# Optimization experiments

Measured on AMD Instinct MI355X. Metric: run time of the kernel, lower is better.

The kernel has to match this reference:

```python
import jax, jax.numpy as jnp
import numpy as np
import math

ALPHA = 0.5


def _dfrft_matrix(N: int, a: float) -> np.ndarray:
    """Candan's discrete fractional Fourier transform matrix (approx order 2),
    as used by torch-frft's dfrft. D(a) = E diag(exp(-i*pi/2*a*k)) E^T, where E
    are eigenvectors (even/odd interleaved, descending eigenvalue) of the
    S = circulant([0,1,0,...,0,1]) + diag(Re fft(s)) matrix that commutes with the DFT.
    Pure numpy; runs at trace time (constants)."""
    s = np.zeros(N)
    s[1] = 1.0
    s[-1] = 1.0
    idx = (np.arange(N)[:, None] - np.arange(N)[None, :]) % N
    S = s[idx] + np.diag(np.fft.fft(s).real)
    # odd/even decomposition matrix P (orthogonal)
    r = N // 2
    even = 1 - (N % 2)
    P = np.zeros((N, N))
    P[0, 0] = 1.0
    c = 1.0 / math.sqrt(2.0)
    for i in range(1, r - even + 1):
        P[i, i] = c
        P[i, N - i] = c
    if even:
        P[r, r] = 1.0
    for i in range(r + 1, N):
        P[i, i] = -c
        P[i, N - i] = c
    CS = P @ S @ P.T
    C2 = CS[: r + 1, : r + 1]
    S2 = CS[r + 1:, r + 1:]
    _, vc = np.linalg.eigh(C2)  # ascending -> reverse for descending order
    _, vs = np.linalg.eigh(S2)
    SC2 = (P @ np.vstack((vc, np.zeros((N - r - 1, r + 1)))))[:, ::-1]  # even evecs
    SS2 = (P @ np.vstack((np.zeros((r + 1, N - r - 1)), vs)))[:, ::-1]  # odd evecs
    if N % 2 == 0:
        E = np.zeros((N, N + 1))
        E[:, 0::2] = SC2
        E[:, 1::2] = np.hstack((SS2, np.zeros((N, 1))))
        E = np.delete(E, N - 1, axis=1)  # skip eigenvalue index N-1, keep N
    else:
        E = np.zeros((N, N))
        E[:, 0::2] = SC2
        E[:, 1::2] = SS2
    shift = 1 - (N % 2)
    k = np.concatenate((np.arange(N - 1), [N - 1 + shift]))
    f = np.exp(-1j * (np.pi / 2.0) * a * k)
    return (E * f[None, :]) @ E.T


def setup_inputs() -> dict:
    key = jax.random.key(0)
    k1, k2, k3, k4, k5 = jax.random.split(key, 5)
    B, Ci, Co, H, W = 16, 64, 64, 128, 128
    scale = 1.0 / Ci
    return {
        "x": jax.random.normal(k1, (B, Ci, H, W), jnp.float32),
        "w_r": jax.random.normal(k2, (Co, Ci), jnp.float32) * scale,
        "w_i": jax.random.normal(k3, (Co, Ci), jnp.float32) * scale,
        "b_r": jax.random.normal(k4, (Co,), jnp.float32) * scale,
        "b_i": jax.random.normal(k5, (Co,), jnp.float32) * scale,
    }


def reference(x, w_r, w_i, b_r, b_i):
    B, Ci, H, W = x.shape
    Aw = jnp.asarray(_dfrft_matrix(W, ALPHA), jnp.complex64)   # dfrft along dim=-1
    Ah = jnp.asarray(_dfrft_matrix(H, ALPHA), jnp.complex64)   # dfrft along dim=-2
    xc = x.astype(jnp.complex64)
    # forward fractional Fourier transforms
    x_ft = jnp.einsum('wv,bchv->bchw', Aw, xc)
    x_ft = jnp.einsum('hg,bcgw->bchw', Ah, x_ft)
    # 1x1 complex conv (complex weight + bias)
    wc = w_r.astype(jnp.complex64) + 1j * w_i.astype(jnp.complex64)
    bc = b_r.astype(jnp.complex64) + 1j * b_i.astype(jnp.complex64)
    out_ft = jnp.einsum('oi,bihw->bohw', wc, x_ft) + bc[None, :, None, None]
    # inverse transforms: D(-a) = conj(D(a)) since eigenvectors are real
    y = jnp.einsum('hg,bogw->bohw', jnp.conj(Ah), out_ft)
    y = jnp.einsum('wv,bohv->bohw', jnp.conj(Aw), y)
    # module returns a complex tensor; expose as stacked (real, imag)
    return jnp.stack((y.real, y.imag), axis=0)
```

## Files before the change

kernel.cpp:

```cpp
#include <hip/hip_runtime.h>
#include <cmath>
#include <cstring>
#include <vector>
#include <algorithm>


struct UV { float ur[128]; float ui[128]; };
static UV g_uv;

namespace {

constexpr int NN = 128;

void matmul_d(const std::vector<double>& A, const std::vector<double>& B,
              std::vector<double>& C, int n) {
  for (int i = 0; i < n; ++i)
    for (int j = 0; j < n; ++j) {
      double s = 0.0;
      for (int k = 0; k < n; ++k) s += A[(size_t)i*n+k] * B[(size_t)k*n+j];
      C[(size_t)i*n+j] = s;
    }
}

void jacobi_eigh(std::vector<double>& A, int n, std::vector<double>& V,
                 std::vector<double>& lam) {
  V.assign((size_t)n*n, 0.0);
  for (int i = 0; i < n; ++i) V[(size_t)i*n+i] = 1.0;
  for (int sweep = 0; sweep < 200; ++sweep) {
    double off = 0.0;
    for (int p = 0; p < n; ++p)
      for (int q = p+1; q < n; ++q) off += A[(size_t)p*n+q]*A[(size_t)p*n+q];
    if (off < 1e-24) break;
    for (int p = 0; p < n-1; ++p)
      for (int q = p+1; q < n; ++q) {
        double apq = A[(size_t)p*n+q];
        if (std::fabs(apq) < 1e-300) continue;
        double app = A[(size_t)p*n+p], aqq = A[(size_t)q*n+q];
        double tau = (aqq - app) / (2.0*apq);
        double t = (tau >= 0 ? 1.0 : -1.0) / (std::fabs(tau) + std::sqrt(1.0 + tau*tau));
        double c = 1.0/std::sqrt(1.0 + t*t), s = t*c;
        for (int k = 0; k < n; ++k) {
          double akp = A[(size_t)k*n+p], akq = A[(size_t)k*n+q];
          A[(size_t)k*n+p] = c*akp - s*akq;
          A[(size_t)k*n+q] = s*akp + c*akq;
        }
        for (int k = 0; k < n; ++k) {
          double apk = A[(size_t)p*n+k], aqk = A[(size_t)q*n+k];
          A[(size_t)p*n+k] = c*apk - s*aqk;
          A[(size_t)q*n+k] = s*apk + c*aqk;
        }
        for (int k = 0; k < n; ++k) {
          double vkp = V[(size_t)k*n+p], vkq = V[(size_t)k*n+q];
          V[(size_t)k*n+p] = c*vkp - s*vkq;
          V[(size_t)k*n+q] = s*vkp + c*vkq;
        }
      }
  }
  lam.resize(n);
  for (int i = 0; i < n; ++i) lam[i] = A[(size_t)i*n+i];
}

bool init_uv() {
  const int n = NN, r = NN/2;
  const double c = 1.0/std::sqrt(2.0);
  const double PI = 3.14159265358979323846;
  std::vector<double> S((size_t)n*n, 0.0), P((size_t)n*n, 0.0);
  for (int i = 0; i < n; ++i) {
    S[(size_t)i*n+i] = 2.0*std::cos(2.0*PI*i/n);
    S[(size_t)i*n + (i+1)%n] += 1.0;
    S[(size_t)i*n + (i-1+n)%n] += 1.0;
  }
  P[0] = 1.0;
  for (int i = 1; i <= r-1; ++i) { P[(size_t)i*n+i] = c;  P[(size_t)i*n + (n-i)] = c; }
  P[(size_t)r*n+r] = 1.0;
  for (int i = r+1; i < n; ++i)  { P[(size_t)i*n+i] = -c; P[(size_t)i*n + (n-i)] = c; }
  std::vector<double> Pt((size_t)n*n), T((size_t)n*n), CS((size_t)n*n);
  for (int i = 0; i < n; ++i)
    for (int j = 0; j < n; ++j) Pt[(size_t)i*n+j] = P[(size_t)j*n+i];
  matmul_d(P, S, T, n);
  matmul_d(T, Pt, CS, n);
  const int m = r + 1;
  std::vector<double> C2((size_t)m*m);
  for (int i = 0; i < m; ++i)
    for (int j = 0; j < m; ++j) C2[(size_t)i*m+j] = CS[(size_t)i*n+j];
  std::vector<double> V, lam;
  jacobi_eigh(C2, m, V, lam);
  std::vector<int> idx(m);
  for (int i = 0; i < m; ++i) idx[i] = i;
  std::sort(idx.begin(), idx.end(), [&](int a, int b){ return lam[a] < lam[b]; });
  double ure[NN] = {0}, uim[NN] = {0};
  for (int mm = 0; mm < m; ++mm) {
    int col = idx[m-1-mm];
    double q[NN];
    q[0] = V[(size_t)0*m+col];
    for (int j = 1; j <= r-1; ++j) q[j] = c * V[(size_t)j*m+col];
    q[r] = V[(size_t)r*m+col];
    for (int j = r+1; j < n; ++j)  q[j] = c * V[(size_t)(n-j)*m+col];
    double ssum = 0.0;
    for (int j = 0; j < n; ++j) ssum += q[j];
    switch (mm & 3) {
      case 0: for (int h = 0; h < n; ++h) ure[h] += q[h]*ssum; break;
      case 1: for (int h = 0; h < n; ++h) uim[h] += q[h]*ssum; break;
      case 2: for (int h = 0; h < n; ++h) ure[h] -= q[h]*ssum; break;
      case 3: for (int h = 0; h < n; ++h) uim[h] -= q[h]*ssum; break;
    }
  }
  for (int h = 0; h < n; ++h) { g_uv.ur[h] = (float)ure[h]; g_uv.ui[h] = (float)uim[h]; }
  return true;
}

bool g_inited = init_uv();

}


__global__ __launch_bounds__(256) void transpose_w_kernel(
    const float* __restrict__ wr, const float* __restrict__ wi,
    float* __restrict__ wTr, float* __restrict__ wTi) {
  int t = blockIdx.x * 256 + threadIdx.x;
  if (t < 4096) {
    int o = t >> 6, i = t & 63;
    wTr[i*64 + o] = wr[t];
    wTi[i*64 + o] = wi[t];
  }
}

__global__ __launch_bounds__(256) void spec_main_kernel(
    const float* __restrict__ x,
    const float* __restrict__ wTr, const float* __restrict__ wTi,
    const float* __restrict__ br, const float* __restrict__ bi,
    float* __restrict__ out, UV uv) {
  __shared__ float xs[64][128];
  const int tid  = threadIdx.x;
  const int bid  = blockIdx.x;
  const int b    = bid >> 7;
  const int hrow = bid & 127;
  const long long pos0 = (long long)hrow << 7;
  const float* xb = x + ((long long)b << 20) + pos0;

#pragma unroll
  for (int k = 0; k < 8; ++k) {
    int q  = tid + (k << 8);
    int i  = q >> 5;
    int pw = (q & 31) << 2;
    float4 v = *(const float4*)(xb + (long long)i * 16384 + pw);
    *(float4*)&xs[i][pw] = v;
  }
  __syncthreads();

  const int lane = tid & 63;
  const int o0   = __builtin_amdgcn_readfirstlane((tid >> 6) << 4);
  const int w0   = lane << 1;

  const float uhr = uv.ur[hrow], uhi = uv.ui[hrow];
  const float v0r = uv.ur[w0],   v0i = uv.ui[w0];
  const float v1r = uv.ur[w0+1], v1i = uv.ui[w0+1];
  const float g0r = uhr*v0r - uhi*v0i, g0i = uhr*v0i + uhi*v0r;
  const float g1r = uhr*v1r - uhi*v1i, g1i = uhr*v1i + uhi*v1r;

  float accr[16][2], acci[16][2];
#pragma unroll
  for (int oo = 0; oo < 16; ++oo) {
    float bro = br[o0+oo], bio = bi[o0+oo];
    accr[oo][0] = bro*g0r - bio*g0i;  acci[oo][0] = bro*g0i + bio*g0r;
    accr[oo][1] = bro*g1r - bio*g1i;  acci[oo][1] = bro*g1i + bio*g1r;
  }

  for (int i = 0; i < 64; ++i) {
    float2 xv = *(const float2*)&xs[i][w0];
    const float* wrp = wTr + (i << 6) + o0;
    const float* wip = wTi + (i << 6) + o0;
#pragma unroll
    for (int oo = 0; oo < 16; ++oo) {
      float wr = wrp[oo], wi = wip[oo];
      accr[oo][0] += wr*xv.x;  accr[oo][1] += wr*xv.y;
      acci[oo][0] += wi*xv.x;  acci[oo][1] += wi*xv.y;
    }
  }

  long long baseR = (((long long)(b*64 + o0)) << 14) + pos0 + w0;
  long long baseI = baseR + ((long long)(16*64) << 14);
#pragma unroll
  for (int oo = 0; oo < 16; ++oo) {
    *(float2*)&out[baseR + ((long long)oo << 14)] = make_float2(accr[oo][0], accr[oo][1]);
    *(float2*)&out[baseI + ((long long)oo << 14)] = make_float2(acci[oo][0], acci[oo][1]);
  }
}

extern "C" void kernel_launch(void* const* d_in, const int* in_sizes, int n_in,
                              void* d_out, int out_size, void* d_ws, size_t ws_size,
                              hipStream_t stream) {
  (void)in_sizes; (void)n_in; (void)out_size; (void)ws_size; (void)g_inited;
  const float* x  = (const float*)d_in[0];
  const float* wr = (const float*)d_in[1];
  const float* wi = (const float*)d_in[2];
  const float* br = (const float*)d_in[3];
  const float* bi = (const float*)d_in[4];
  float* out = (float*)d_out;
  float* wTr = (float*)d_ws;
  float* wTi = wTr + 4096;

  transpose_w_kernel<<<16, 256, 0, stream>>>(wr, wi, wTr, wTi);
  spec_main_kernel<<<2048, 256, 0, stream>>>(x, wTr, wTi, br, bi, out, g_uv);
}
```

Before: 212.2 us.

## Drop LDS staging, read x directly with register prefetch, use 512-thread blocks

Removes the shared-memory tile and the block barrier. Each thread now loads its own x values straight from global memory and prefetches the next two input channels into registers while it computes on the current ones. Blocks grow to 512 threads, each wave covering 8 output channels instead of 16, which lowers register pressure and raises occupancy. The cost is that each x element is now read from global memory by 8 waves instead of once per block, relying on cache hits, and loop unrolling is reduced.

```diff
diff --git a/kernel.cpp b/kernel.cpp
--- a/kernel.cpp
+++ b/kernel.cpp
@@ -125,32 +125,20 @@
   }
 }
 
-__global__ __launch_bounds__(256) void spec_main_kernel(
+__global__ __launch_bounds__(512, 8) void spec_main_kernel(
     const float* __restrict__ x,
     const float* __restrict__ wTr, const float* __restrict__ wTi,
     const float* __restrict__ br, const float* __restrict__ bi,
     float* __restrict__ out, UV uv) {
-  __shared__ float xs[64][128];
   const int tid  = threadIdx.x;
   const int bid  = blockIdx.x;
   const int b    = bid >> 7;
   const int hrow = bid & 127;
+  const int lane = tid & 63;
+  const int o0   = __builtin_amdgcn_readfirstlane((tid >> 6) << 3);
+  const int w0   = lane << 1;
   const long long pos0 = (long long)hrow << 7;
-  const float* xb = x + ((long long)b << 20) + pos0;
-
-#pragma unroll
-  for (int k = 0; k < 8; ++k) {
-    int q  = tid + (k << 8);
-    int i  = q >> 5;
-    int pw = (q & 31) << 2;
-    float4 v = *(const float4*)(xb + (long long)i * 16384 + pw);
-    *(float4*)&xs[i][pw] = v;
-  }
-  __syncthreads();
-
-  const int lane = tid & 63;
-  const int o0   = __builtin_amdgcn_readfirstlane((tid >> 6) << 4);
-  const int w0   = lane << 1;
+  const float* xp = x + ((long long)b << 20) + pos0 + w0;
 
   const float uhr = uv.ur[hrow], uhi = uv.ui[hrow];
   const float v0r = uv.ur[w0],   v0i = uv.ui[w0];
@@ -158,30 +146,43 @@
   const float g0r = uhr*v0r - uhi*v0i, g0i = uhr*v0i + uhi*v0r;
   const float g1r = uhr*v1r - uhi*v1i, g1i = uhr*v1i + uhi*v1r;
 
-  float accr[16][2], acci[16][2];
-#pragma unroll
-  for (int oo = 0; oo < 16; ++oo) {
+  float accr[8][2], acci[8][2];
+#pragma unroll
+  for (int oo = 0; oo < 8; ++oo) {
     float bro = br[o0+oo], bio = bi[o0+oo];
     accr[oo][0] = bro*g0r - bio*g0i;  acci[oo][0] = bro*g0i + bio*g0r;
     accr[oo][1] = bro*g1r - bio*g1i;  acci[oo][1] = bro*g1i + bio*g1r;
   }
 
-  for (int i = 0; i < 64; ++i) {
-    float2 xv = *(const float2*)&xs[i][w0];
-    const float* wrp = wTr + (i << 6) + o0;
-    const float* wip = wTi + (i << 6) + o0;
-#pragma unroll
-    for (int oo = 0; oo < 16; ++oo) {
-      float wr = wrp[oo], wi = wip[oo];
-      accr[oo][0] += wr*xv.x;  accr[oo][1] += wr*xv.y;
-      acci[oo][0] += wi*xv.x;  acci[oo][1] += wi*xv.y;
-    }
+  float2 c0 = *(const float2*)(xp);
+  float2 c1 = *(const float2*)(xp + 16384);
+#pragma unroll 1
+  for (int i = 0; i < 64; i += 2) {
+    const int p0 = (i + 2 < 64) ? i + 2 : 63;
+    const int p1 = (i + 3 < 64) ? i + 3 : 63;
+    float2 n0 = *(const float2*)(xp + ((long long)p0 << 14));
+    float2 n1 = *(const float2*)(xp + ((long long)p1 << 14));
+    const float* wr0 = wTr + (i << 6) + o0;
+    const float* wi0 = wTi + (i << 6) + o0;
+#pragma unroll
+    for (int oo = 0; oo < 8; ++oo) {
+      float wr = wr0[oo], wi = wi0[oo];
+      accr[oo][0] += wr*c0.x;  accr[oo][1] += wr*c0.y;
+      acci[oo][0] += wi*c0.x;  acci[oo][1] += wi*c0.y;
+    }
+#pragma unroll
+    for (int oo = 0; oo < 8; ++oo) {
+      float wr = wr0[64+oo], wi = wi0[64+oo];
+      accr[oo][0] += wr*c1.x;  accr[oo][1] += wr*c1.y;
+      acci[oo][0] += wi*c1.x;  acci[oo][1] += wi*c1.y;
+    }
+    c0 = n0; c1 = n1;
   }
 
   long long baseR = (((long long)(b*64 + o0)) << 14) + pos0 + w0;
   long long baseI = baseR + ((long long)(16*64) << 14);
 #pragma unroll
-  for (int oo = 0; oo < 16; ++oo) {
+  for (int oo = 0; oo < 8; ++oo) {
     *(float2*)&out[baseR + ((long long)oo << 14)] = make_float2(accr[oo][0], accr[oo][1]);
     *(float2*)&out[baseI + ((long long)oo << 14)] = make_float2(acci[oo][0], acci[oo][1]);
   }
@@ -201,5 +202,5 @@
   float* wTi = wTr + 4096;
 
   transpose_w_kernel<<<16, 256, 0, stream>>>(wr, wi, wTr, wTi);
-  spec_main_kernel<<<2048, 256, 0, stream>>>(x, wTr, wTi, br, bi, out, g_uv);
-}
+  spec_main_kernel<<<2048, 512, 0, stream>>>(x, wTr, wTi, br, bi, out, g_uv);
+}
```

After: 225.5 us. +6.2%, slower.
